# Optimization experiments

Measured on AMD Instinct MI355X. Metric: run time of the kernel, lower is better.

The kernel has to match this reference:

```python
import jax, jax.numpy as jnp
import numpy as np

H = 256        # hidden_dim == num_features
C = 10         # num_classes
N = 100000     # nodes
E = 1600000    # edges
BN_EPS = 1e-5
NEG_SLOPE = 0.1


def _bn(h, gamma, beta):
    # training-mode BatchNorm1d over node dim, biased variance (torch semantics)
    mu = jnp.mean(h, axis=0)
    var = jnp.mean(jnp.square(h - mu), axis=0)
    return (h - mu) * jax.lax.rsqrt(var + BN_EPS) * gamma + beta


def setup_inputs() -> dict:
    key = jax.random.key(0)
    ks = jax.random.split(key, 12)
    s = 1.0 / np.sqrt(H)
    x = jax.random.normal(ks[0], (N, H), dtype=jnp.float32)
    edge_index = jax.random.randint(ks[1], (2, E), 0, N, dtype=jnp.int64)
    return {
        "x": x,
        "edge_index": edge_index,
        # GIN MLP: lin1 -> bn -> relu -> lin2
        "W1": jax.random.uniform(ks[2], (H, H), jnp.float32, -s, s),
        "b1": jnp.zeros((H,), jnp.float32),
        "g_mlp": jnp.ones((H,), jnp.float32),
        "be_mlp": jnp.zeros((H,), jnp.float32),
        "W2": jax.random.uniform(ks[3], (H, H), jnp.float32, -s, s),
        "b2": jnp.zeros((H,), jnp.float32),
        # bn4
        "g4": jnp.ones((H,), jnp.float32),
        "be4": jnp.zeros((H,), jnp.float32),
        # head
        "Wl1": jax.random.uniform(ks[4], (H, H // 2), jnp.float32, -s, s),
        "bl1": jnp.zeros((H // 2,), jnp.float32),
        "Wl3": jax.random.uniform(ks[5], (H // 2, C), jnp.float32, -s, s),
        "bl3": jnp.zeros((C,), jnp.float32),
    }


def reference(x, edge_index, W1, b1, g_mlp, be_mlp, W2, b2, g4, be4, Wl1, bl1, Wl3, bl3):
    lrelu = lambda h: jax.nn.leaky_relu(h, NEG_SLOPE)
    src, dst = edge_index[0], edge_index[1]
    # GINConv: sum-aggregate neighbor messages (source_to_target), eps=0
    agg = jax.ops.segment_sum(x[src], dst, num_segments=x.shape[0])  # [N,H]
    h = agg + x  # (1+eps)*x + sum
    # PyG MLP([H,H,H]): lin -> batch_norm -> relu -> lin (plain last)
    h = jax.nn.relu(_bn(h @ W1 + b1, g_mlp, be_mlp)) @ W2 + b2
    x1 = lrelu(h)                     # relu(conv1(...), 0.1); dropout p=0
    h = lrelu(x1)                     # relu(x1, 0.1)
    h = lrelu(_bn(h, g4, be4))        # relu(bn4(x), 0.1); dropout p=0
    h = x + 0.01 * h                  # residual with original features
    h = lrelu(h @ Wl1 + bl1)
    return h @ Wl3 + bl3              # [N, C]
```

## Files before the change

kernel.cpp:

```cpp
#include <hip/hip_runtime.h>

constexpr int NN = 100000;
constexpr int NE = 1600000;
constexpr int HD = 256;
constexpr int NBUCK = 782;
constexpr int CGRID = 98;

typedef __attribute__((ext_vector_type(4))) float  f32x4;
typedef __attribute__((ext_vector_type(2))) float  f32x2;
typedef __attribute__((ext_vector_type(8))) short  bf16x8;

#if defined(__has_builtin)
#if __has_builtin(__builtin_amdgcn_cvt_pk_f32_fp8) && __has_builtin(__builtin_amdgcn_cvt_pk_fp8_f32)
#define HAVE_FP8_CVT 1
#endif
#endif
#ifndef HAVE_FP8_CVT
#define HAVE_FP8_CVT 0
#endif

__device__ __forceinline__ float bf2f(unsigned short u) {
  union { unsigned int i; float f; } c;
  c.i = ((unsigned int)u) << 16;
  return c.f;
}
__device__ __forceinline__ short f2bf(float f) {
  union { float f; unsigned int i; } c; c.f = f;
  unsigned int i = c.i + 0x7fffu + ((c.i >> 16) & 1u);
  return (short)(i >> 16);
}

__device__ __forceinline__ void gload16(const void* g, void* l) {
  __builtin_amdgcn_global_load_lds(
      (const __attribute__((address_space(1))) unsigned int*)g,
      (__attribute__((address_space(3))) unsigned int*)l, 16, 0, 0);
}

__global__ void k_detect(const int* __restrict__ ew, int* __restrict__ flag) {
  __shared__ int bad;
  if (threadIdx.x == 0) bad = 0;
  __syncthreads();
  int nz = 0;
  for (int i = threadIdx.x; i < 2048; i += 256) nz |= ew[2 * i + 1];
  if (nz) atomicOr(&bad, 1);
  __syncthreads();
  if (threadIdx.x == 0) *flag = (bad == 0) ? 1 : 0;
}

__global__ void k_cvtW(const float* __restrict__ W1, const float* __restrict__ W2,
                       const float* __restrict__ Wl1, short* __restrict__ W1T,
                       short* __restrict__ W2T, short* __restrict__ Wl1T) {
  int b = blockIdx.x, t = threadIdx.x;
  if (b < 256)       W1T[b * 256 + t]        = f2bf(W1[t * 256 + b]);
  else if (b < 512){ int n = b - 256; W2T[n * 256 + t]  = f2bf(W2[t * 256 + n]); }
  else             { int n = b - 512; Wl1T[n * 256 + t] = f2bf(Wl1[t * 128 + n]); }
}

#if HAVE_FP8_CVT
__global__ void k_cvtX(const float* __restrict__ x, void* __restrict__ xq) {
  int c = blockIdx.x * 256 + threadIdx.x;
  float4 a = ((const float4*)x)[2 * (size_t)c];
  float4 b = ((const float4*)x)[2 * (size_t)c + 1];
  int p0 = 0, p1 = 0;
  p0 = __builtin_amdgcn_cvt_pk_fp8_f32(a.x, a.y, p0, false);
  p0 = __builtin_amdgcn_cvt_pk_fp8_f32(a.z, a.w, p0, true);
  p1 = __builtin_amdgcn_cvt_pk_fp8_f32(b.x, b.y, p1, false);
  p1 = __builtin_amdgcn_cvt_pk_fp8_f32(b.z, b.w, p1, true);
  ((int2*)xq)[c] = make_int2(p0, p1);
}
#else
__global__ void k_cvtX(const float* __restrict__ x, void* __restrict__ xq) {
  int c = blockIdx.x * 256 + threadIdx.x;
  float4 a = ((const float4*)x)[2 * (size_t)c];
  float4 b = ((const float4*)x)[2 * (size_t)c + 1];
  bf16x8 o;
  o[0] = f2bf(a.x); o[1] = f2bf(a.y); o[2] = f2bf(a.z); o[3] = f2bf(a.w);
  o[4] = f2bf(b.x); o[5] = f2bf(b.y); o[6] = f2bf(b.z); o[7] = f2bf(b.w);
  ((bf16x8*)xq)[c] = o;
}
#endif

__global__ __launch_bounds__(1024) void k_count(const int* __restrict__ ew,
                                                const int* __restrict__ flag,
                                                int* __restrict__ cntmat) {
  __shared__ int lcnt[NBUCK];
  int m64 = *flag;
  int t = threadIdx.x;
  for (int i = t; i < NBUCK; i += 1024) lcnt[i] = 0;
  __syncthreads();
  int base = blockIdx.x * 16384;
#pragma unroll
  for (int u = 0; u < 16; u++) {
    int e = base + u * 1024 + t;
    if (e < NE) {
      int d = m64 ? ew[2 * (NE + e)] : ew[NE + e];
      atomicAdd(&lcnt[d >> 7], 1);
    }
  }
  __syncthreads();
  for (int i = t; i < NBUCK; i += 1024) cntmat[blockIdx.x * NBUCK + i] = lcnt[i];
}

__global__ __launch_bounds__(1024) void k_colscan(int* __restrict__ cntmat,
                                                  int* __restrict__ bases,
                                                  int* __restrict__ off_) {
  __shared__ int tot[1024];
  int t = threadIdx.x;
  int sum = 0;
  if (t < NBUCK) {
    for (int g = 0; g < CGRID; g++) sum += cntmat[g * NBUCK + t];
    tot[t] = sum;
  }
  __syncthreads();
  int v = (t < NBUCK) ? sum : 0;
  for (int o = 1; o < 1024; o <<= 1) {
    int u = (t >= o && t < NBUCK) ? tot[t - o] : 0;
    __syncthreads();
    if (t < NBUCK) tot[t] += u;
    __syncthreads();
  }
  if (t < NBUCK) {
    int b = tot[t] - v;
    bases[t] = b;
    int run = b;
    for (int g = 0; g < CGRID; g++) {
      int c = cntmat[g * NBUCK + t];
      cntmat[g * NBUCK + t] = run;
      run += c;
    }
  }
  if (t == NBUCK) bases[NBUCK] = NE;
  if (t == NBUCK + 1) off_[NN] = NE;
}

__global__ __launch_bounds__(1024) void k_scatter(const int* __restrict__ ew,
                                                  const int* __restrict__ flag,
                                                  const int* __restrict__ cntmat,
                                                  int* __restrict__ pairs) {
  __shared__ int lcur[NBUCK];
  int m64 = *flag;
  int t = threadIdx.x;
  for (int i = t; i < NBUCK; i += 1024) lcur[i] = cntmat[blockIdx.x * NBUCK + i];
  __syncthreads();
  int base = blockIdx.x * 16384;
#pragma unroll
  for (int u = 0; u < 16; u++) {
    int e = base + u * 1024 + t;
    if (e < NE) {
      int d = m64 ? ew[2 * (NE + e)] : ew[NE + e];
      int s = m64 ? ew[2 * e] : ew[e];
      int slot = atomicAdd(&lcur[d >> 7], 1);
      pairs[slot] = s | ((d & 127) << 17);
    }
  }
}

__global__ __launch_bounds__(256) void k_bsort(const int* __restrict__ pairs,
                                               const int* __restrict__ bases,
                                               int* __restrict__ off_,
                                               int* __restrict__ csr) {
  __shared__ int lcnt[128], lofs[128], lcur[128];
  int b = blockIdx.x, t = threadIdx.x;
  int s0 = bases[b], s1 = bases[b + 1];
  if (t < 128) lcnt[t] = 0;
  __syncthreads();
  for (int j = s0 + t; j < s1; j += 256) atomicAdd(&lcnt[(pairs[j] >> 17) & 127], 1);
  __syncthreads();
  int v = (t < 128) ? lcnt[t] : 0;
  if (t < 128) lofs[t] = v;
  __syncthreads();
  for (int o = 1; o < 128; o <<= 1) {
    int u = (t >= o && t < 128) ? lofs[t - o] : 0;
    __syncthreads();
    if (t < 128) lofs[t] += u;
    __syncthreads();
  }
  if (t < 128) {
    int ex = lofs[t] - v;
    lcur[t] = ex;
    int node = b * 128 + t;
    if (node < NN) off_[node] = s0 + ex;
  }
  __syncthreads();
  for (int j = s0 + t; j < s1; j += 256) {
    int p = pairs[j];
    int slot = atomicAdd(&lcur[(p >> 17) & 127], 1);
    csr[s0 + slot] = p & 0x1FFFF;
  }
}

#if HAVE_FP8_CVT
__global__ __launch_bounds__(256) void k_agg2(const void* __restrict__ xq,
                                              const int* __restrict__ off_,
                                              const int* __restrict__ csr,
                                              short* __restrict__ h0) {
  int node = blockIdx.x * 4 + (threadIdx.x >> 6);
  int lane = threadIdx.x & 63;
  const unsigned char* xb = (const unsigned char*)xq;
  size_t boff = (size_t)lane * 4;
  int s0 = off_[node], s1 = off_[node + 1];
  int sw = *(const int*)(xb + (size_t)node * 256 + boff);
  f32x2 slo = __builtin_amdgcn_cvt_pk_f32_fp8(sw, false);
  f32x2 shi = __builtin_amdgcn_cvt_pk_f32_fp8(sw, true);
  float a0 = slo[0], a1 = slo[1], a2 = shi[0], a3 = shi[1];
  int j = s0;
  while (j + 8 <= s1) {
    int idx[8];
#pragma unroll
    for (int u = 0; u < 8; u++) idx[u] = csr[j + u];
    int w[8];
#pragma unroll
    for (int u = 0; u < 8; u++) w[u] = *(const int*)(xb + (size_t)idx[u] * 256 + boff);
#pragma unroll
    for (int u = 0; u < 8; u++) {
      f32x2 lo = __builtin_amdgcn_cvt_pk_f32_fp8(w[u], false);
      f32x2 hi = __builtin_amdgcn_cvt_pk_f32_fp8(w[u], true);
      a0 += lo[0]; a1 += lo[1]; a2 += hi[0]; a3 += hi[1];
    }
    j += 8;
  }
  if (j + 4 <= s1) {
    int idx[4];
#pragma unroll
    for (int u = 0; u < 4; u++) idx[u] = csr[j + u];
    int w[4];
#pragma unroll
    for (int u = 0; u < 4; u++) w[u] = *(const int*)(xb + (size_t)idx[u] * 256 + boff);
#pragma unroll
    for (int u = 0; u < 4; u++) {
      f32x2 lo = __builtin_amdgcn_cvt_pk_f32_fp8(w[u], false);
      f32x2 hi = __builtin_amdgcn_cvt_pk_f32_fp8(w[u], true);
      a0 += lo[0]; a1 += lo[1]; a2 += hi[0]; a3 += hi[1];
    }
    j += 4;
  }
  for (; j < s1; j++) {
    int s = csr[j];
    int w = *(const int*)(xb + (size_t)s * 256 + boff);
    f32x2 lo = __builtin_amdgcn_cvt_pk_f32_fp8(w, false);
    f32x2 hi = __builtin_amdgcn_cvt_pk_f32_fp8(w, true);
    a0 += lo[0]; a1 += lo[1]; a2 += hi[0]; a3 += hi[1];
  }
  ushort4 o;
  o.x = (ushort)f2bf(a0); o.y = (ushort)f2bf(a1);
  o.z = (ushort)f2bf(a2); o.w = (ushort)f2bf(a3);
  *(ushort4*)((ushort*)h0 + (size_t)node * 256 + (size_t)lane * 4) = o;
}
#else
__global__ __launch_bounds__(256) void k_agg2(const void* __restrict__ xq,
                                              const int* __restrict__ off_,
                                              const int* __restrict__ csr,
                                              short* __restrict__ h0) {
  int node = blockIdx.x * 4 + (threadIdx.x >> 6);
  int lane = threadIdx.x & 63;
  const ushort* xu = (const ushort*)xq;
  size_t coff = (size_t)lane * 4;
  int s0 = off_[node], s1 = off_[node + 1];
  ushort4 sv = *(const ushort4*)(xu + (size_t)node * 256 + coff);
  float a0 = bf2f(sv.x), a1 = bf2f(sv.y), a2 = bf2f(sv.z), a3 = bf2f(sv.w);
  int j = s0;
  while (j + 8 <= s1) {
    int idx[8];
#pragma unroll
    for (int u = 0; u < 8; u++) idx[u] = csr[j + u];
    ushort4 v[8];
#pragma unroll
    for (int u = 0; u < 8; u++) v[u] = *(const ushort4*)(xu + (size_t)idx[u] * 256 + coff);
#pragma unroll
    for (int u = 0; u < 8; u++) {
      a0 += bf2f(v[u].x); a1 += bf2f(v[u].y);
      a2 += bf2f(v[u].z); a3 += bf2f(v[u].w);
    }
    j += 8;
  }
  for (; j < s1; j++) {
    int s = csr[j];
    ushort4 v = *(const ushort4*)(xu + (size_t)s * 256 + coff);
    a0 += bf2f(v.x); a1 += bf2f(v.y); a2 += bf2f(v.z); a3 += bf2f(v.w);
  }
  ushort4 o;
  o.x = (ushort)f2bf(a0); o.y = (ushort)f2bf(a1);
  o.z = (ushort)f2bf(a2); o.w = (ushort)f2bf(a3);
  *(ushort4*)((ushort*)h0 + (size_t)node * 256 + coff) = o;
}
#endif

template <int ACT, int TIN, int STATS>
__global__ __launch_bounds__(256, 2) void k_gemm(const short* __restrict__ A,
                                              const short* __restrict__ BT,
                                              const float* __restrict__ bias,
                                              short* __restrict__ C, int M,
                                              const float* __restrict__ tsc,
                                              const float* __restrict__ tsh,
                                              float* __restrict__ gsum,
                                              float* __restrict__ gssq) {
  __shared__ char smem[65536];
  __shared__ float lsc[256], lsh[256];
  __shared__ float lsum[128], lssq[128];
  int tid = threadIdx.x;
  int lane = tid & 63, w = tid >> 6;
  if (TIN) { lsc[tid] = tsc[tid]; lsh[tid] = tsh[tid]; }
  if (STATS && tid < 128) { lsum[tid] = 0.f; lssq[tid] = 0.f; }
  int bm = blockIdx.x >> 1, bn = blockIdx.x & 1;
  int bm0 = bm * 128, bn0 = bn * 128;
  int wm = w >> 1, wn = w & 1;
  int lr = lane & 15, lg = lane >> 4;
  f32x4 acc[4][4] = {};
  __syncthreads();

  bf16x8 stg[4];

#pragma unroll 1
  for (int it = 0; it < 4; ++it) {
    int b = it & 1;
    if (it == 0) {
      if (TIN) {
#pragma unroll
        for (int i = 0; i < 4; ++i) {
          int p = tid + 256 * i, row = p >> 3, s = (p & 7) ^ (row & 7);
          int grow = bm0 + row; if (grow > M - 1) grow = M - 1;
          stg[i] = *(const bf16x8*)(A + (size_t)grow * 256 + s * 8);
        }
      } else {
#pragma unroll
        for (int q = 0; q < 4; ++q) {
          int wc = w * 4 + q;
          int p = wc * 64 + lane, row = p >> 3, s = (p & 7) ^ (row & 7);
          int grow = bm0 + row; if (grow > M - 1) grow = M - 1;
          gload16(A + (size_t)grow * 256 + s * 8, smem + wc * 1024);
        }
      }
#pragma unroll
      for (int q = 0; q < 4; ++q) {
        int wc = w * 4 + q;
        int p = wc * 64 + lane, row = p >> 3, s = (p & 7) ^ (row & 7);
        gload16(BT + (size_t)(bn0 + row) * 256 + s * 8, smem + 16384 + wc * 1024);
      }
      if (TIN) {
#pragma unroll
        for (int i = 0; i < 4; ++i) {
          int p = tid + 256 * i, row = p >> 3, s = (p & 7) ^ (row & 7);
          int k0 = s * 8;
          float4 sc0 = *(const float4*)&lsc[k0], sc1 = *(const float4*)&lsc[k0 + 4];
          float4 sh0 = *(const float4*)&lsh[k0], sh1 = *(const float4*)&lsh[k0 + 4];
          bf16x8 v = stg[i], o;
          o[0] = f2bf(fmaxf(bf2f((unsigned short)v[0]) * sc0.x + sh0.x, 0.f));
          o[1] = f2bf(fmaxf(bf2f((unsigned short)v[1]) * sc0.y + sh0.y, 0.f));
          o[2] = f2bf(fmaxf(bf2f((unsigned short)v[2]) * sc0.z + sh0.z, 0.f));
          o[3] = f2bf(fmaxf(bf2f((unsigned short)v[3]) * sc0.w + sh0.w, 0.f));
          o[4] = f2bf(fmaxf(bf2f((unsigned short)v[4]) * sc1.x + sh1.x, 0.f));
          o[5] = f2bf(fmaxf(bf2f((unsigned short)v[5]) * sc1.y + sh1.y, 0.f));
          o[6] = f2bf(fmaxf(bf2f((unsigned short)v[6]) * sc1.z + sh1.z, 0.f));
          o[7] = f2bf(fmaxf(bf2f((unsigned short)v[7]) * sc1.w + sh1.w, 0.f));
          *(bf16x8*)(smem + p * 16) = o;
        }
      }
      __syncthreads();
    }
    int ktn = (it + 1) * 64;
    if (it < 3) {
      char* nb = smem + (b ^ 1) * 32768;
      if (TIN) {
#pragma unroll
        for (int i = 0; i < 4; ++i) {
          int p = tid + 256 * i, row = p >> 3, s = (p & 7) ^ (row & 7);
          int grow = bm0 + row; if (grow > M - 1) grow = M - 1;
          stg[i] = *(const bf16x8*)(A + (size_t)grow * 256 + ktn + s * 8);
        }
      } else {
#pragma unroll
        for (int q = 0; q < 4; ++q) {
          int wc = w * 4 + q;
          int p = wc * 64 + lane, row = p >> 3, s = (p & 7) ^ (row & 7);
          int grow = bm0 + row; if (grow > M - 1) grow = M - 1;
          gload16(A + (size_t)grow * 256 + ktn + s * 8, nb + wc * 1024);
        }
      }
#pragma unroll
      for (int q = 0; q < 4; ++q) {
        int wc = w * 4 + q;
        int p = wc * 64 + lane, row = p >> 3, s = (p & 7) ^ (row & 7);
        gload16(BT + (size_t)(bn0 + row) * 256 + ktn + s * 8, nb + 16384 + wc * 1024);
      }
    }
    const char* sa = smem + b * 32768;
    const char* sb = sa + 16384;
#pragma unroll
    for (int ks = 0; ks < 2; ++ks) {
      bf16x8 af[4], bfr[4];
#pragma unroll
      for (int mi = 0; mi < 4; ++mi) {
        int row = wm * 64 + mi * 16 + lr;
        int q = (lg + 4 * ks) ^ (row & 7);
        af[mi] = *(const bf16x8*)(sa + row * 128 + q * 16);
      }
#pragma unroll
      for (int ni = 0; ni < 4; ++ni) {
        int row = wn * 64 + ni * 16 + lr;
        int q = (lg + 4 * ks) ^ (row & 7);
        bfr[ni] = *(const bf16x8*)(sb + row * 128 + q * 16);
      }
#pragma unroll
      for (int mi = 0; mi < 4; ++mi)
#pragma unroll
        for (int ni = 0; ni < 4; ++ni)
          acc[mi][ni] = __builtin_amdgcn_mfma_f32_16x16x32_bf16(af[mi], bfr[ni], acc[mi][ni], 0, 0, 0);
    }
    if (TIN && it < 3) {
      char* nb = smem + (b ^ 1) * 32768;
#pragma unroll
      for (int i = 0; i < 4; ++i) {
        int p = tid + 256 * i, row = p >> 3, s = (p & 7) ^ (row & 7);
        int k0 = ktn + s * 8;
        float4 sc0 = *(const float4*)&lsc[k0], sc1 = *(const float4*)&lsc[k0 + 4];
        float4 sh0 = *(const float4*)&lsh[k0], sh1 = *(const float4*)&lsh[k0 + 4];
        bf16x8 v = stg[i], o;
        o[0] = f2bf(fmaxf(bf2f((unsigned short)v[0]) * sc0.x + sh0.x, 0.f));
        o[1] = f2bf(fmaxf(bf2f((unsigned short)v[1]) * sc0.y + sh0.y, 0.f));
        o[2] = f2bf(fmaxf(bf2f((unsigned short)v[2]) * sc0.z + sh0.z, 0.f));
        o[3] = f2bf(fmaxf(bf2f((unsigned short)v[3]) * sc0.w + sh0.w, 0.f));
        o[4] = f2bf(fmaxf(bf2f((unsigned short)v[4]) * sc1.x + sh1.x, 0.f));
        o[5] = f2bf(fmaxf(bf2f((unsigned short)v[5]) * sc1.y + sh1.y, 0.f));
        o[6] = f2bf(fmaxf(bf2f((unsigned short)v[6]) * sc1.z + sh1.z, 0.f));
        o[7] = f2bf(fmaxf(bf2f((unsigned short)v[7]) * sc1.w + sh1.w, 0.f));
        *(bf16x8*)(nb + p * 16) = o;
      }
    }
    __syncthreads();
  }

  short* zs = (short*)smem;
#pragma unroll
  for (int ni = 0; ni < 4; ++ni) {
    int col = wn * 64 + ni * 16 + lr;
    float bv = bias[bn0 + col];
    float ps = 0.f, pq = 0.f;
#pragma unroll
    for (int mi = 0; mi < 4; ++mi) {
#pragma unroll
      for (int r = 0; r < 4; ++r) {
        int row = wm * 64 + mi * 16 + lg * 4 + r;
        float tv = acc[mi][ni][r] + bv;
        if (ACT == 1) tv = tv > 0.f ? tv : 0.01f * tv;
        if (STATS && (bm0 + row) < M) { ps += tv; pq += tv * tv; }
        zs[row * 136 + col] = f2bf(tv);
      }
    }
    if (STATS) {
      ps += __shfl_xor(ps, 16); pq += __shfl_xor(pq, 16);
      ps += __shfl_xor(ps, 32); pq += __shfl_xor(pq, 32);
      if (lane < 16) {
        atomicAdd(&lsum[wn * 64 + ni * 16 + lane], ps);
        atomicAdd(&lssq[wn * 64 + ni * 16 + lane], pq);
      }
    }
  }
  __syncthreads();
  {
    int row = tid >> 1;
    int grow = bm0 + row;
    if (grow < M) {
#pragma unroll
      for (int i = 0; i < 8; ++i) {
        int cs = (tid & 1) * 8 + i;
        bf16x8 v = *(const bf16x8*)((const char*)zs + row * 272 + cs * 16);
        *(bf16x8*)(C + (size_t)grow * 256 + bn0 + cs * 8) = v;
      }
    }
  }
  if (STATS) {
    if (tid < 128) {
      atomicAdd(&gsum[bn0 + tid], lsum[tid]);
      atomicAdd(&gssq[bn0 + tid], lssq[tid]);
    }
  }
}

__global__ void k_bnprep(const float* __restrict__ sum, const float* __restrict__ ssq,
                         const float* __restrict__ g, const float* __restrict__ be,
                         float* __restrict__ scale, float* __restrict__ shift, int M) {
  int c = threadIdx.x;
  float mu = sum[c] / (float)M;
  float var = ssq[c] / (float)M - mu * mu;
  float rs = rsqrtf(var + 1e-5f);
  float sc = g[c] * rs;
  scale[c] = sc;
  shift[c] = be[c] - mu * sc;
}

__global__ __launch_bounds__(256) void k_head(const short* __restrict__ V,
                                              const float* __restrict__ x,
                                              const short* __restrict__ BT,
                                              const float* __restrict__ bl1,
                                              const float* __restrict__ Wl3,
                                              const float* __restrict__ bl3,
                                              const float* __restrict__ tsc,
                                              const float* __restrict__ tsh,
                                              float* __restrict__ out, int M) {
  __shared__ char smem[128 * 140 * 2 + 1280 * 4];
  __shared__ float lsc[256], lsh[256];
  short* zs  = (short*)smem;
  float* wl3 = (float*)(smem + 128 * 140 * 2);
  short* ldsA = (short*)smem;
  short* ldsB = (short*)smem + 4096;
  int tid = threadIdx.x;
  for (int i = tid; i < 1280; i += 256) wl3[i] = Wl3[i];
  lsc[tid] = tsc[tid]; lsh[tid] = tsh[tid];
  __syncthreads();
  int bm0 = blockIdx.x * 128;
  int lane = tid & 63, w = tid >> 6;
  int wm = w >> 1, wn = w & 1;
  int lr = lane & 15, lg = lane >> 4;
  f32x4 acc[4][4] = {};
  for (int kt = 0; kt < 256; kt += 32) {
#pragma unroll
    for (int c = 0; c < 2; c++) {
      int chunk = c * 256 + tid;
      int row = chunk >> 2;
      int kc = (chunk & 3) * 8;
      int rA = bm0 + row; if (rA > M - 1) rA = M - 1;
      bf16x8 va = *(const bf16x8*)(V + (size_t)rA * 256 + kt + kc);
      float4 x0 = *(const float4*)(x + (size_t)rA * 256 + kt + kc);
      float4 x1 = *(const float4*)(x + (size_t)rA * 256 + kt + kc + 4);
      float xs[8] = {x0.x, x0.y, x0.z, x0.w, x1.x, x1.y, x1.z, x1.w};
      bf16x8 tt;
#pragma unroll
      for (int jj = 0; jj < 8; jj++) {
        float f = bf2f((unsigned short)va[jj]) * lsc[kt + kc + jj] + lsh[kt + kc + jj];
        f = f > 0.f ? f : 0.1f * f;
        tt[jj] = f2bf(xs[jj] + 0.01f * f);
      }
      *((bf16x8*)ldsA + chunk) = tt;
      *((bf16x8*)ldsB + chunk) = *(const bf16x8*)(BT + (size_t)row * 256 + kt + kc);
    }
    __syncthreads();
    bf16x8 af[4], bfr[4];
#pragma unroll
    for (int mi = 0; mi < 4; mi++) af[mi] = *((const bf16x8*)ldsA + ((wm * 64 + mi * 16 + lr) * 4 + lg));
#pragma unroll
    for (int ni = 0; ni < 4; ni++) bfr[ni] = *((const bf16x8*)ldsB + ((wn * 64 + ni * 16 + lr) * 4 + lg));
#pragma unroll
    for (int mi = 0; mi < 4; mi++)
#pragma unroll
      for (int ni = 0; ni < 4; ni++)
        acc[mi][ni] = __builtin_amdgcn_mfma_f32_16x16x32_bf16(af[mi], bfr[ni], acc[mi][ni], 0, 0, 0);
    __syncthreads();
  }
#pragma unroll
  for (int ni = 0; ni < 4; ni++) {
    int col = wn * 64 + ni * 16 + lr;
    float bv = bl1[col];
#pragma unroll
    for (int mi = 0; mi < 4; mi++) {
#pragma unroll
      for (int r = 0; r < 4; r++) {
        int rl = wm * 64 + mi * 16 + lg * 4 + r;
        float tv = acc[mi][ni][r] + bv;
        tv = tv > 0.f ? tv : 0.1f * tv;
        zs[rl * 140 + col] = f2bf(tv);
      }
    }
  }
  __syncthreads();
  int r = tid >> 1, ch = tid & 1;
  float av[5];
#pragma unroll
  for (int c = 0; c < 5; c++) av[c] = bl3[ch * 5 + c];
  for (int k = 0; k < 128; k++) {
    float zv = bf2f((unsigned short)zs[r * 140 + k]);
#pragma unroll
    for (int c = 0; c < 5; c++) av[c] += zv * wl3[k * 10 + ch * 5 + c];
  }
  int grow = bm0 + r;
  if (grow < M) {
#pragma unroll
    for (int c = 0; c < 5; c++) out[(size_t)grow * 10 + ch * 5 + c] = av[c];
  }
}

extern "C" void kernel_launch(void* const* d_in, const int* in_sizes, int n_in,
                              void* d_out, int out_size, void* d_ws, size_t ws_size,
                              hipStream_t stream) {
  const float* x   = (const float*)d_in[0];
  const int*   ew  = (const int*)d_in[1];
  const float* W1  = (const float*)d_in[2];
  const float* b1  = (const float*)d_in[3];
  const float* g1  = (const float*)d_in[4];
  const float* be1 = (const float*)d_in[5];
  const float* W2  = (const float*)d_in[6];
  const float* b2  = (const float*)d_in[7];
  const float* g4  = (const float*)d_in[8];
  const float* be4 = (const float*)d_in[9];
  const float* Wl1 = (const float*)d_in[10];
  const float* bl1 = (const float*)d_in[11];
  const float* Wl3 = (const float*)d_in[12];
  const float* bl3 = (const float*)d_in[13];
  float* out = (float*)d_out;

  char* ws = (char*)d_ws;
  const size_t OFF_OFF  = 0;
  const size_t OFF_BASES= 400128;
  const size_t OFF_CNT  = 800256;
  const size_t OFF_STATS= 1200384;
  const size_t OFF_BN   = 1204480;
  const size_t OFF_FLAG = 1208576;
  const size_t OFF_W1T  = 1209216;
  const size_t OFF_W2T  = 1340288;
  const size_t OFF_WL1T = 1471360;
  const size_t OFF_CSR  = 1536896;
  const size_t OFF_BUFA = 7936896;
  const size_t OFF_BUFB = 59136896;
  if (ws_size < 110336896) return;

  int* off_  = (int*)(ws + OFF_OFF);
  int* bases_= (int*)(ws + OFF_BASES);
  int* cnt_  = (int*)(ws + OFF_CNT);
  float* sum1 = (float*)(ws + OFF_STATS);
  float* ssq1 = sum1 + 256;
  float* sum4 = sum1 + 512;
  float* ssq4 = sum1 + 768;
  float* sc1 = (float*)(ws + OFF_BN);
  float* sh1 = sc1 + 256;
  float* sc4 = sc1 + 512;
  float* sh4 = sc1 + 768;
  int* flag_ = (int*)(ws + OFF_FLAG);
  short* W1T  = (short*)(ws + OFF_W1T);
  short* W2T  = (short*)(ws + OFF_W2T);
  short* Wl1T = (short*)(ws + OFF_WL1T);
  int* csr_   = (int*)(ws + OFF_CSR);
  short* bufA = (short*)(ws + OFF_BUFA);
  short* bufB = (short*)(ws + OFF_BUFB);
  int* pairs_ = (int*)(ws + OFF_BUFA);
  void* xq    = (void*)bufB;

  hipMemsetAsync(ws + OFF_STATS, 0, 4096, stream);
  k_detect<<<1, 256, 0, stream>>>(ew, flag_);
  k_cvtW<<<640, 256, 0, stream>>>(W1, W2, Wl1, W1T, W2T, Wl1T);
  k_cvtX<<<12500, 256, 0, stream>>>(x, xq);
  k_count<<<CGRID, 1024, 0, stream>>>(ew, flag_, cnt_);
  k_colscan<<<1, 1024, 0, stream>>>(cnt_, bases_, off_);
  k_scatter<<<CGRID, 1024, 0, stream>>>(ew, flag_, cnt_, pairs_);
  k_bsort<<<NBUCK, 256, 0, stream>>>(pairs_, bases_, off_, csr_);
  k_agg2<<<25000, 256, 0, stream>>>(xq, off_, csr_, bufA);
  k_gemm<0, 0, 1><<<1564, 256, 0, stream>>>(bufA, W1T, b1, bufB, NN,
                                            nullptr, nullptr, sum1, ssq1);
  k_bnprep<<<1, 256, 0, stream>>>(sum1, ssq1, g1, be1, sc1, sh1, NN);
  k_gemm<1, 1, 1><<<1564, 256, 0, stream>>>(bufB, W2T, b2, bufA, NN,
                                            sc1, sh1, sum4, ssq4);
  k_bnprep<<<1, 256, 0, stream>>>(sum4, ssq4, g4, be4, sc4, sh4, NN);
  k_head<<<782, 256, 0, stream>>>(bufA, x, Wl1T, bl1, Wl3, bl3, sc4, sh4, out, NN);
}
```

Baseline: 303.9 us.

## Double-buffer head GEMM with swizzled LDS and MFMA final projection

Restructures the head kernel to use 64-wide K steps with double-buffered LDS. Next-tile global loads and async B loads overlap the MFMA work, and an XOR swizzle avoids bank conflicts. The scalar 128x10 output projection is replaced by an MFMA using a bf16 transposed, zero-padded Wl3 prepared in the weight conversion kernel. This adds 64KB LDS per block and bf16 rounding of the final layer's weights.

```diff
diff --git a/kernel.cpp b/kernel.cpp
--- a/kernel.cpp
+++ b/kernel.cpp
@@ -48,12 +48,20 @@
 }
 
 __global__ void k_cvtW(const float* __restrict__ W1, const float* __restrict__ W2,
-                       const float* __restrict__ Wl1, short* __restrict__ W1T,
-                       short* __restrict__ W2T, short* __restrict__ Wl1T) {
+                       const float* __restrict__ Wl1, const float* __restrict__ Wl3,
+                       short* __restrict__ W1T, short* __restrict__ W2T,
+                       short* __restrict__ Wl1T, short* __restrict__ Wl3T) {
   int b = blockIdx.x, t = threadIdx.x;
   if (b < 256)       W1T[b * 256 + t]        = f2bf(W1[t * 256 + b]);
   else if (b < 512){ int n = b - 256; W2T[n * 256 + t]  = f2bf(W2[t * 256 + n]); }
-  else             { int n = b - 512; Wl1T[n * 256 + t] = f2bf(Wl1[t * 128 + n]); }
+  else if (b < 640){ int n = b - 512; Wl1T[n * 256 + t] = f2bf(Wl1[t * 128 + n]); }
+  else {
+    if (t < 128) {
+#pragma unroll
+      for (int c = 0; c < 16; ++c)
+        Wl3T[c * 128 + t] = (c < 10) ? f2bf(Wl3[t * 10 + c]) : (short)0;
+    }
+  }
 }
 
 #if HAVE_FP8_CVT
@@ -488,93 +496,169 @@
   shift[c] = be[c] - mu * sc;
 }
 
-__global__ __launch_bounds__(256) void k_head(const short* __restrict__ V,
-                                              const float* __restrict__ x,
-                                              const short* __restrict__ BT,
-                                              const float* __restrict__ bl1,
-                                              const float* __restrict__ Wl3,
-                                              const float* __restrict__ bl3,
-                                              const float* __restrict__ tsc,
-                                              const float* __restrict__ tsh,
-                                              float* __restrict__ out, int M) {
-  __shared__ char smem[128 * 140 * 2 + 1280 * 4];
+__global__ __launch_bounds__(256, 2) void k_head(const short* __restrict__ V,
+                                                 const float* __restrict__ x,
+                                                 const short* __restrict__ BT,
+                                                 const float* __restrict__ bl1,
+                                                 const short* __restrict__ wl3t,
+                                                 const float* __restrict__ bl3,
+                                                 const float* __restrict__ tsc,
+                                                 const float* __restrict__ tsh,
+                                                 float* __restrict__ out, int M) {
+  __shared__ char smem[65536];
   __shared__ float lsc[256], lsh[256];
-  short* zs  = (short*)smem;
-  float* wl3 = (float*)(smem + 128 * 140 * 2);
-  short* ldsA = (short*)smem;
-  short* ldsB = (short*)smem + 4096;
+  __shared__ short wl3s[2048];
   int tid = threadIdx.x;
-  for (int i = tid; i < 1280; i += 256) wl3[i] = Wl3[i];
+  int lane = tid & 63, w = tid >> 6;
   lsc[tid] = tsc[tid]; lsh[tid] = tsh[tid];
-  __syncthreads();
+  {
+    int p = w * 64 + lane;
+    gload16(wl3t + (size_t)p * 8, (char*)wl3s + w * 1024);
+  }
   int bm0 = blockIdx.x * 128;
-  int lane = tid & 63, w = tid >> 6;
   int wm = w >> 1, wn = w & 1;
   int lr = lane & 15, lg = lane >> 4;
   f32x4 acc[4][4] = {};
-  for (int kt = 0; kt < 256; kt += 32) {
-#pragma unroll
-    for (int c = 0; c < 2; c++) {
-      int chunk = c * 256 + tid;
-      int row = chunk >> 2;
-      int kc = (chunk & 3) * 8;
-      int rA = bm0 + row; if (rA > M - 1) rA = M - 1;
-      bf16x8 va = *(const bf16x8*)(V + (size_t)rA * 256 + kt + kc);
-      float4 x0 = *(const float4*)(x + (size_t)rA * 256 + kt + kc);
-      float4 x1 = *(const float4*)(x + (size_t)rA * 256 + kt + kc + 4);
-      float xs[8] = {x0.x, x0.y, x0.z, x0.w, x1.x, x1.y, x1.z, x1.w};
-      bf16x8 tt;
-#pragma unroll
-      for (int jj = 0; jj < 8; jj++) {
-        float f = bf2f((unsigned short)va[jj]) * lsc[kt + kc + jj] + lsh[kt + kc + jj];
-        f = f > 0.f ? f : 0.1f * f;
-        tt[jj] = f2bf(xs[jj] + 0.01f * f);
-      }
-      *((bf16x8*)ldsA + chunk) = tt;
-      *((bf16x8*)ldsB + chunk) = *(const bf16x8*)(BT + (size_t)row * 256 + kt + kc);
+  __syncthreads();
+
+  bf16x8 stgv[4];
+  float stgx[4][8];
+
+#pragma unroll 1
+  for (int it = 0; it < 4; ++it) {
+    int b = it & 1;
+    if (it == 0) {
+#pragma unroll
+      for (int i = 0; i < 4; ++i) {
+        int p = tid + 256 * i, row = p >> 3, s = (p & 7) ^ (row & 7);
+        int grow = bm0 + row; if (grow > M - 1) grow = M - 1;
+        size_t base = (size_t)grow * 256 + s * 8;
+        stgv[i] = *(const bf16x8*)(V + base);
+        *(float4*)&stgx[i][0] = *(const float4*)(x + base);
+        *(float4*)&stgx[i][4] = *(const float4*)(x + base + 4);
+      }
+#pragma unroll
+      for (int q = 0; q < 4; ++q) {
+        int wc = w * 4 + q;
+        int p = wc * 64 + lane, row = p >> 3, s = (p & 7) ^ (row & 7);
+        gload16(BT + (size_t)row * 256 + s * 8, smem + 16384 + wc * 1024);
+      }
+#pragma unroll
+      for (int i = 0; i < 4; ++i) {
+        int p = tid + 256 * i, row = p >> 3, s = (p & 7) ^ (row & 7);
+        int k0 = s * 8;
+        bf16x8 v = stgv[i], o;
+#pragma unroll
+        for (int jj = 0; jj < 8; ++jj) {
+          float f = bf2f((unsigned short)v[jj]) * lsc[k0 + jj] + lsh[k0 + jj];
+          f = f > 0.f ? f : 0.1f * f;
+          o[jj] = f2bf(stgx[i][jj] + 0.01f * f);
+        }
+        *(bf16x8*)(smem + p * 16) = o;
+      }
+      __syncthreads();
+    }
+    int ktn = (it + 1) * 64;
+    if (it < 3) {
+      char* nb = smem + (b ^ 1) * 32768;
+#pragma unroll
+      for (int i = 0; i < 4; ++i) {
+        int p = tid + 256 * i, row = p >> 3, s = (p & 7) ^ (row & 7);
+        int grow = bm0 + row; if (grow > M - 1) grow = M - 1;
+        size_t base = (size_t)grow * 256 + ktn + s * 8;
+        stgv[i] = *(const bf16x8*)(V + base);
+        *(float4*)&stgx[i][0] = *(const float4*)(x + base);
+        *(float4*)&stgx[i][4] = *(const float4*)(x + base + 4);
+      }
+#pragma unroll
+      for (int q = 0; q < 4; ++q) {
+        int wc = w * 4 + q;
+        int p = wc * 64 + lane, row = p >> 3, s = (p & 7) ^ (row & 7);
+        gload16(BT + (size_t)row * 256 + ktn + s * 8, nb + 16384 + wc * 1024);
+      }
+    }
+    const char* sa = smem + b * 32768;
+    const char* sb = sa + 16384;
+#pragma unroll
+    for (int ks = 0; ks < 2; ++ks) {
+      bf16x8 af[4], bfr[4];
+#pragma unroll
+      for (int mi = 0; mi < 4; ++mi) {
+        int row = wm * 64 + mi * 16 + lr;
+        int q = (lg + 4 * ks) ^ (row & 7);
+        af[mi] = *(const bf16x8*)(sa + row * 128 + q * 16);
+      }
+#pragma unroll
+      for (int ni = 0; ni < 4; ++ni) {
+        int row = wn * 64 + ni * 16 + lr;
+        int q = (lg + 4 * ks) ^ (row & 7);
+        bfr[ni] = *(const bf16x8*)(sb + row * 128 + q * 16);
+      }
+#pragma unroll
+      for (int mi = 0; mi < 4; ++mi)
+#pragma unroll
+        for (int ni = 0; ni < 4; ++ni)
+          acc[mi][ni] = __builtin_amdgcn_mfma_f32_16x16x32_bf16(af[mi], bfr[ni], acc[mi][ni], 0, 0, 0);
+    }
+    if (it < 3) {
+      char* nb = smem + (b ^ 1) * 32768;
+#pragma unroll
+      for (int i = 0; i < 4; ++i) {
+        int p = tid + 256 * i, row = p >> 3, s = (p & 7) ^ (row & 7);
+        int k0 = ktn + s * 8;
+        bf16x8 v = stgv[i], o;
+#pragma unroll
+        for (int jj = 0; jj < 8; ++jj) {
+          float f = bf2f((unsigned short)v[jj]) * lsc[k0 + jj] + lsh[k0 + jj];
+          f = f > 0.f ? f : 0.1f * f;
+          o[jj] = f2bf(stgx[i][jj] + 0.01f * f);
+        }
+        *(bf16x8*)(nb + p * 16) = o;
+      }
     }
     __syncthreads();
-    bf16x8 af[4], bfr[4];
-#pragma unroll
-    for (int mi = 0; mi < 4; mi++) af[mi] = *((const bf16x8*)ldsA + ((wm * 64 + mi * 16 + lr) * 4 + lg));
-#pragma unroll
-    for (int ni = 0; ni < 4; ni++) bfr[ni] = *((const bf16x8*)ldsB + ((wn * 64 + ni * 16 + lr) * 4 + lg));
-#pragma unroll
-    for (int mi = 0; mi < 4; mi++)
-#pragma unroll
-      for (int ni = 0; ni < 4; ni++)
-        acc[mi][ni] = __builtin_amdgcn_mfma_f32_16x16x32_bf16(af[mi], bfr[ni], acc[mi][ni], 0, 0, 0);
-    __syncthreads();
-  }
-#pragma unroll
-  for (int ni = 0; ni < 4; ni++) {
+  }
+
+  short* zs = (short*)smem;
+#pragma unroll
+  for (int ni = 0; ni < 4; ++ni) {
     int col = wn * 64 + ni * 16 + lr;
     float bv = bl1[col];
 #pragma unroll
-    for (int mi = 0; mi < 4; mi++) {
-#pragma unroll
-      for (int r = 0; r < 4; r++) {
-        int rl = wm * 64 + mi * 16 + lg * 4 + r;
+    for (int mi = 0; mi < 4; ++mi) {
+#pragma unroll
+      for (int r = 0; r < 4; ++r) {
+        int row = wm * 64 + mi * 16 + lg * 4 + r;
         float tv = acc[mi][ni][r] + bv;
         tv = tv > 0.f ? tv : 0.1f * tv;
-        zs[rl * 140 + col] = f2bf(tv);
-      }
-    }
-  }
-  __syncthreads();
-  int r = tid >> 1, ch = tid & 1;
-  float av[5];
-#pragma unroll
-  for (int c = 0; c < 5; c++) av[c] = bl3[ch * 5 + c];
-  for (int k = 0; k < 128; k++) {
-    float zv = bf2f((unsigned short)zs[r * 140 + k]);
-#pragma unroll
-    for (int c = 0; c < 5; c++) av[c] += zv * wl3[k * 10 + ch * 5 + c];
-  }
-  int grow = bm0 + r;
-  if (grow < M) {
-#pragma unroll
-    for (int c = 0; c < 5; c++) out[(size_t)grow * 10 + ch * 5 + c] = av[c];
+        zs[row * 136 + col] = f2bf(tv);
+      }
+    }
+  }
+  __syncthreads();
+
+  f32x4 acc2[2] = {};
+#pragma unroll
+  for (int kk = 0; kk < 4; ++kk) {
+    bf16x8 bfr = *(const bf16x8*)((const char*)wl3s + lr * 256 + (kk * 4 + lg) * 16);
+#pragma unroll
+    for (int m = 0; m < 2; ++m) {
+      int row = (w * 2 + m) * 16 + lr;
+      bf16x8 af = *(const bf16x8*)((const char*)zs + row * 272 + (kk * 4 + lg) * 16);
+      acc2[m] = __builtin_amdgcn_mfma_f32_16x16x32_bf16(af, bfr, acc2[m], 0, 0, 0);
+    }
+  }
+  if (lr < 10) {
+    float bv = bl3[lr];
+#pragma unroll
+    for (int m = 0; m < 2; ++m) {
+#pragma unroll
+      for (int r = 0; r < 4; ++r) {
+        int row = (w * 2 + m) * 16 + lg * 4 + r;
+        int grow = bm0 + row;
+        if (grow < M) out[(size_t)grow * 10 + lr] = acc2[m][r] + bv;
+      }
+    }
   }
 }
 
@@ -601,6 +685,7 @@
   const size_t OFF_OFF  = 0;
   const size_t OFF_BASES= 400128;
   const size_t OFF_CNT  = 800256;
+  const size_t OFF_WL3T = 1106944;
   const size_t OFF_STATS= 1200384;
   const size_t OFF_BN   = 1204480;
   const size_t OFF_FLAG = 1208576;
@@ -627,6 +712,7 @@
   short* W1T  = (short*)(ws + OFF_W1T);
   short* W2T  = (short*)(ws + OFF_W2T);
   short* Wl1T = (short*)(ws + OFF_WL1T);
+  short* Wl3T = (short*)(ws + OFF_WL3T);
   int* csr_   = (int*)(ws + OFF_CSR);
   short* bufA = (short*)(ws + OFF_BUFA);
   short* bufB = (short*)(ws + OFF_BUFB);
@@ -635,7 +721,7 @@
 
   hipMemsetAsync(ws + OFF_STATS, 0, 4096, stream);
   k_detect<<<1, 256, 0, stream>>>(ew, flag_);
-  k_cvtW<<<640, 256, 0, stream>>>(W1, W2, Wl1, W1T, W2T, Wl1T);
+  k_cvtW<<<641, 256, 0, stream>>>(W1, W2, Wl1, Wl3, W1T, W2T, Wl1T, Wl3T);
   k_cvtX<<<12500, 256, 0, stream>>>(x, xq);
   k_count<<<CGRID, 1024, 0, stream>>>(ew, flag_, cnt_);
   k_colscan<<<1, 1024, 0, stream>>>(cnt_, bases_, off_);
@@ -648,5 +734,5 @@
   k_gemm<1, 1, 1><<<1564, 256, 0, stream>>>(bufB, W2T, b2, bufA, NN,
                                             sc1, sh1, sum4, ssq4);
   k_bnprep<<<1, 256, 0, stream>>>(sum4, ssq4, g4, be4, sc4, sh4, NN);
-  k_head<<<782, 256, 0, stream>>>(bufA, x, Wl1T, bl1, Wl3, bl3, sc4, sh4, out, NN);
-}
+  k_head<<<782, 256, 0, stream>>>(bufA, x, Wl1T, bl1, Wl3T, bl3, sc4, sh4, out, NN);
+}
```

Result: no change. 300.4 us (-1.1%).
